# Kernel optimization log

Measured on AMD Instinct MI355X. Metric: run time of the kernel, lower is better.

## Reference

```python
import jax, jax.numpy as jnp
import numpy as np

DIM, M_DIM, FOURIER, KNN = 128, 16, 4, 32
EDGE_IN = 2 * FOURIER + 2 * DIM + 1  # 265


def silu(x):
    return x * jax.nn.sigmoid(x)


def setup_inputs() -> dict:
    key = jax.random.key(0)
    ks = jax.random.split(key, 12)
    b, n = 2, 4096

    def w(k, shape):
        return jax.random.normal(k, shape, dtype=jnp.float32) * 0.02

    return {
        "feats": jax.random.normal(ks[0], (b, n, DIM), dtype=jnp.float32),
        "coors": jax.random.normal(ks[1], (b, n, 3), dtype=jnp.float32) * 3.0,
        # edge_mlp: Linear(265, 530) -> SiLU -> Linear(530, 16) -> SiLU
        "We1": w(ks[2], (EDGE_IN, 2 * EDGE_IN)), "be1": jnp.zeros((2 * EDGE_IN,), jnp.float32),
        "We2": w(ks[3], (2 * EDGE_IN, M_DIM)), "be2": jnp.zeros((M_DIM,), jnp.float32),
        # coors_mlp: Linear(16, 64) -> SiLU -> Linear(64, 1)
        "Wc1": w(ks[4], (M_DIM, 4 * M_DIM)), "bc1": jnp.zeros((4 * M_DIM,), jnp.float32),
        "Wc2": w(ks[5], (4 * M_DIM, 1)), "bc2": jnp.zeros((1,), jnp.float32),
        # node_mlp: Linear(dim+16, 2*dim) -> SiLU -> Linear(2*dim, dim)
        "Wn1": w(ks[6], (DIM + M_DIM, 2 * DIM)), "bn1": jnp.zeros((2 * DIM,), jnp.float32),
        "Wn2": w(ks[7], (2 * DIM, DIM)), "bn2": jnp.zeros((DIM,), jnp.float32),
    }


def reference(feats, coors, We1, be1, We2, be2, Wc1, bc1, Wc2, bc2, Wn1, bn1, Wn2, bn2):
    b, n, d = feats.shape
    # pairwise relative coords and squared distance: (b, n, n, 3), (b, n, n)
    rel_coors = coors[:, :, None, :] - coors[:, None, :, :]
    rel_dist = jnp.sum(rel_coors ** 2, axis=-1)

    # k nearest neighbors (smallest distance)
    _, idx = jax.lax.top_k(-rel_dist, KNN)  # (b, n, K)
    rel_coors = jnp.take_along_axis(rel_coors, idx[..., None], axis=2)  # (b, n, K, 3)
    rel_dist = jnp.take_along_axis(rel_dist, idx, axis=2)[..., None]    # (b, n, K, 1)

    # fourier encode distance -> (b, n, K, 2*F + 1)
    scales = 2.0 ** jnp.arange(FOURIER, dtype=rel_dist.dtype)
    xs = rel_dist[..., None] / scales  # (b, n, K, 1, F)
    fe = jnp.concatenate([jnp.sin(xs), jnp.cos(xs), rel_dist[..., None]], axis=-1)
    rel_dist = fe.reshape(b, n, KNN, 2 * FOURIER + 1)

    bidx = jnp.arange(b)[:, None, None]
    feats_j = feats[bidx, idx]                                   # (b, n, K, d)
    feats_i = jnp.broadcast_to(feats[:, :, None, :], (b, n, KNN, d))

    edge_in = jnp.concatenate([feats_i, feats_j, rel_dist], axis=-1)  # (b, n, K, 265)
    m_ij = silu(silu(edge_in @ We1 + be1) @ We2 + be2)                # (b, n, K, m)

    coor_w = (silu(m_ij @ Wc1 + bc1) @ Wc2 + bc2)[..., 0]             # (b, n, K)
    coors_out = jnp.einsum('bij,bijc->bic', coor_w, rel_coors) + coors

    m_i = m_ij.sum(axis=2)                                            # (b, n, m)
    node_h = silu(jnp.concatenate([feats, m_i], axis=-1) @ Wn1 + bn1)
    node_out = node_h @ Wn2 + bn2 + feats
    return node_out, coors_out
```

## Files before the change

### kernel.cpp

```cpp
#include <hip/hip_runtime.h>
#include <hip/hip_bf16.h>
#include <stdint.h>

typedef __hip_bfloat16 bf16;

using sh8    = __attribute__((ext_vector_type(8)))  short;
using sh4    = __attribute__((ext_vector_type(4)))  short;
using us4    = __attribute__((ext_vector_type(4)))  unsigned short;
using f32x16 = __attribute__((ext_vector_type(16))) float;
using fx4    = __attribute__((ext_vector_type(4)))  float;
using i32x2  = __attribute__((ext_vector_type(2)))  int;

#define NN    4096
#define NODES 8192
#define DIM   128
#define MD    16
#define KNNK  32
#define H1N   530
#define CPAD  544
#define PROW  1088

#define OFF_W1AB 0
#define OFF_WE2A 8704
#define OFF_WC1A 17536
#define OFF_BE2  19584
#define OFF_BC1  19616
#define OFF_WC2  19744
#define OFF_BC2  19872
#define WIMG_SH  19880

__device__ __forceinline__ float b2f(bf16 x){ return __bfloat162float(x); }
__device__ __forceinline__ bf16  f2b(float x){ return __float2bfloat16(x); }
__device__ __forceinline__ float silu_f(float x){
    return x * __builtin_amdgcn_rcpf(1.f + __expf(-x));
}

__device__ __forceinline__ unsigned short f2us(float f){
    unsigned x = __float_as_uint(f);
    unsigned r = x + 0x7FFFu + ((x >> 16) & 1u);
    return (unsigned short)(r >> 16);
}
__device__ __forceinline__ float us2f(unsigned short u){
    return __uint_as_float(((unsigned)u) << 16);
}
__device__ __forceinline__ unsigned pkbf(float a, float b){
    __hip_bfloat162 v = __float22bfloat162_rn(make_float2(a, b));
    return *(unsigned*)&v;
}
__device__ __forceinline__ void plswap(unsigned &a, unsigned &b){
    i32x2 r = __builtin_amdgcn_permlane32_swap((int)a, (int)b, false, false);
    a = (unsigned)r[0]; b = (unsigned)r[1];
}
__device__ __forceinline__ sh8 mk8(unsigned a, unsigned b, unsigned c, unsigned d){
    union { unsigned u[4]; sh8 s; } x;
    x.u[0] = a; x.u[1] = b; x.u[2] = c; x.u[3] = d;
    return x.s;
}
__device__ __forceinline__ float ldconv(const void* p, int fl, size_t i){
    return fl ? ((const float*)p)[i] : b2f(((const bf16*)p)[i]);
}

struct Ptrs { const void* p[14]; int n[14]; };

__global__ __launch_bounds__(256) void detect_kernel(Ptrs ps, int* flags){
    int tn = blockIdx.x;
    const bf16* s = (const bf16*)ps.p[tn];
    int n = ps.n[tn]; if (n > 8192) n = 8192;
    int bad = 0;
    for (int i = threadIdx.x; i < n; i += 256){
        float v = b2f(s[i]);
        if (!(fabsf(v) <= 64.f)) bad = 1;
    }
    __shared__ int sbad;
    if (threadIdx.x == 0) sbad = 0;
    __syncthreads();
    if (bad) atomicOr(&sbad, 1);
    __syncthreads();
    if (threadIdx.x == 0) flags[tn] = sbad;
}

#define PREP_TOTAL 1315776
__global__ __launch_bounds__(256) void prep_all(Ptrs ps, const int* __restrict__ flags,
        unsigned short* __restrict__ gwimg, unsigned short* __restrict__ We1T,
        unsigned short* __restrict__ fBF,   float* __restrict__ coorsF,
        float* __restrict__ be1F,  float* __restrict__ Wn1F,
        float* __restrict__ bn1F,  float* __restrict__ Wn2F,
        float* __restrict__ bn2F){
    int gid = blockIdx.x * 256 + threadIdx.x;
    if (gid < 4352){
        int c = gid >> 3, f = gid & 7;
        gwimg[OFF_W1AB + gid] =
            (c < H1N) ? f2us(ldconv(ps.p[2], flags[2], (size_t)(256 + f) * H1N + c)) : 0;
    } else if (gid < 8704){
        int e = gid - 4352; int c = e >> 3, jj = e & 7;
        gwimg[OFF_W1AB + 4352 + e] =
            (jj == 0 && c < H1N) ? f2us(ldconv(ps.p[2], flags[2], (size_t)264 * H1N + c)) : 0;
    } else if (gid < 17536){
        int e = gid - 8704; int o = e / 552, c = e - o * 552;
        gwimg[OFF_WE2A + e] =
            (c < H1N) ? f2us(ldconv(ps.p[4], flags[4], (size_t)c * 16 + o)) : 0;
    } else if (gid < 19584){
        int e = gid - 17536; int u = e >> 5, k = e & 31;
        gwimg[OFF_WC1A + e] =
            (k < 16) ? f2us(ldconv(ps.p[6], flags[6], (size_t)k * 64 + u)) : 0;
    } else if (gid < 19600){
        ((float*)(gwimg + OFF_BE2))[gid - 19584] = ldconv(ps.p[5], flags[5], gid - 19584);
    } else if (gid < 19664){
        ((float*)(gwimg + OFF_BC1))[gid - 19600] = ldconv(ps.p[7], flags[7], gid - 19600);
    } else if (gid < 19728){
        ((float*)(gwimg + OFF_WC2))[gid - 19664] = ldconv(ps.p[8], flags[8], gid - 19664);
    } else if (gid < 19732){
        int z = gid - 19728;
        ((float*)(gwimg + OFF_BC2))[z] = (z == 0) ? ldconv(ps.p[9], flags[9], 0) : 0.f;
    } else if (gid >= 32768 && gid < 172032){
        int e = gid - 32768; int n = e >> 7, k = e & 127;
        float v;
        if (n < CPAD) v = (n < H1N) ? ldconv(ps.p[2], flags[2], (size_t)k * H1N + n) : 0.f;
        else { int n2 = n - CPAD;
               v = (n2 < H1N) ? ldconv(ps.p[2], flags[2], (size_t)(128 + k) * H1N + n2) : 0.f; }
        We1T[e] = f2us(v);
    } else if (gid >= 172032 && gid < 1220608){
        int e = gid - 172032;
        fBF[e] = f2us(ldconv(ps.p[0], flags[0], e));
    } else if (gid >= 1220608 && gid < 1245184){
        int e = gid - 1220608;
        coorsF[e] = ldconv(ps.p[1], flags[1], e);
    } else if (gid >= 1245184 && gid < 1245714){
        int e = gid - 1245184;
        be1F[e] = ldconv(ps.p[3], flags[3], e);
    } else if (gid >= 1245760 && gid < 1282624){
        int e = gid - 1245760;
        Wn1F[e] = ldconv(ps.p[10], flags[10], e);
    } else if (gid >= 1282624 && gid < 1282880){
        int e = gid - 1282624;
        bn1F[e] = ldconv(ps.p[11], flags[11], e);
    } else if (gid >= 1282880 && gid < 1315648){
        int e = gid - 1282880;
        Wn2F[e] = ldconv(ps.p[12], flags[12], e);
    } else if (gid >= 1315648 && gid < 1315776){
        int e = gid - 1315648;
        bn2F[e] = ldconv(ps.p[13], flags[13], e);
    }
}

__global__ __launch_bounds__(512, 6) void knn_pgemm(
        const float* __restrict__ coors, int* __restrict__ idx_out,
        const unsigned short* __restrict__ fBF,
        const unsigned short* __restrict__ We1T,
        const float* __restrict__ be1, unsigned short* __restrict__ P){
    __shared__ unsigned hist[8][1024];
    __shared__ unsigned long long blist[8][64];
    __shared__ int cntO[8], cntB[8];

    int bid = blockIdx.x;
    int t = threadIdx.x, lane = t & 63, wid = t >> 6;
    int e31 = lane & 31, hi = lane >> 5;

    bool is_knn = (bid < 2048) && !(bid & 1);
    int sub = (bid < 2048) ? (bid >> 1) : (bid - 1024);

    if (!is_knn){
        int bx = sub & 63, by = sub >> 6;
        int mW = (bx << 7) + ((wid & 3) << 5);
        int n0 = (by << 6) + ((wid >> 2) << 5);

        const unsigned short* Arow = fBF  + (size_t)(mW + e31) * DIM + hi * 8;
        const unsigned short* Brow = We1T + (size_t)(n0 + e31) * DIM + hi * 8;

        f32x16 acc = {0.f,0.f,0.f,0.f,0.f,0.f,0.f,0.f,0.f,0.f,0.f,0.f,0.f,0.f,0.f,0.f};
        #pragma unroll
        for (int kc = 0; kc < 8; ++kc){
            sh8 a  = *(const sh8*)(Arow + kc * 16);
            sh8 bv = *(const sh8*)(Brow + kc * 16);
            acc = __builtin_amdgcn_mfma_f32_32x32x16_bf16(a, bv, acc, 0, 0, 0);
        }
        int n = n0 + e31;
        float beadd = 0.f;
        if (n < CPAD) beadd = (n < H1N) ? be1[n] : 0.f;
        #pragma unroll
        for (int g = 0; g < 4; ++g)
            #pragma unroll
            for (int r = 0; r < 4; ++r){
                int m = mW + 8*g + 4*hi + r;
                P[(size_t)m * PROW + n] = f2us(acc[4*g + r] + beadd);
            }
        return;
    }

    int node = (sub << 3) + wid;
    int b = node >> 12, i = node & (NN - 1);
    const float* cb = coors + (size_t)b * NN * 3;

    float qx = cb[i*3+0], qy = cb[i*3+1], qz = cb[i*3+2];

    unsigned* h = &hist[wid][0];
    {
        uint4* hz = (uint4*)h;
        uint4 z = make_uint4(0,0,0,0);
        #pragma unroll
        for (int zl = 0; zl < 4; ++zl) hz[zl * 64 + lane] = z;
    }
    if (lane == 0){ cntO[wid] = 0; cntB[wid] = 0; }
    asm volatile("" ::: "memory");

    #pragma unroll 4
    for (int s = 0; s < 64; ++s){
        int j = (s << 6) + lane;
        float dx = qx - cb[j*3+0];
        float dy = qy - cb[j*3+1];
        float dz = qz - cb[j*3+2];
        float d  = dx*dx + dy*dy + dz*dz;
        float d2 = d * d;
        atomicAdd(&h[__float_as_uint(d2 * d2) >> 22], 1u);
    }
    asm volatile("s_waitcnt lgkmcnt(0)" ::: "memory");

    unsigned S = 0;
    {
        uint4* hz = (uint4*)h;
        #pragma unroll
        for (int g = 0; g < 4; ++g){
            uint4 v = hz[lane * 4 + g];
            S += v.x + v.y + v.z + v.w;
        }
    }
    unsigned scan = S;
    #pragma unroll
    for (int off = 1; off < 64; off <<= 1){
        unsigned nv = __shfl_up(scan, off);
        if (lane >= off) scan += nv;
    }
    unsigned excl = scan - S;
    unsigned long long own = __ballot(excl < KNNK && excl + S >= KNNK);
    int src = __ffsll((unsigned long long)own) - 1;
    unsigned run = excl, Bloc = 0, below_l = 0;
    #pragma unroll
    for (int r = 0; r < 16; ++r){
        unsigned c = h[lane * 16 + r];
        if (run < KNNK && run + c >= KNNK){ Bloc = lane * 16 + r; below_l = run; }
        run += c;
    }
    unsigned B    = __shfl(Bloc, src);
    unsigned below= __shfl(below_l, src);
    unsigned need = KNNK - below;

    int* co = &cntO[wid];
    int* cbn = &cntB[wid];
    unsigned long long* bl = &blist[wid][0];
    #pragma unroll 4
    for (int s = 0; s < 64; ++s){
        int j = (s << 6) + lane;
        float dx = qx - cb[j*3+0];
        float dy = qy - cb[j*3+1];
        float dz = qz - cb[j*3+2];
        float d  = dx*dx + dy*dy + dz*dz;
        float d2 = d * d;
        unsigned bk = __float_as_uint(d2 * d2) >> 22;
        if (bk < B){
            int pos = atomicAdd(co, 1);
            idx_out[(size_t)node * KNNK + pos] = j;
        } else if (bk == B){
            unsigned long long mk = ((unsigned long long)__float_as_uint(d) << 32)
                                    | (unsigned)j;
            int p = atomicAdd(cbn, 1);
            if (p < 64) bl[p] = mk;
        }
    }
    asm volatile("s_waitcnt lgkmcnt(0) vmcnt(0)" ::: "memory");
    int nb = *cbn;

    if (nb <= 64){
        unsigned long long e = (lane < nb) ? bl[lane] : ~0ull;
        for (unsigned r = 0; r < need; ++r){
            unsigned long long m = e;
            #pragma unroll
            for (int off = 32; off > 0; off >>= 1){
                unsigned long long o = __shfl_xor(m, off);
                if (o < m) m = o;
            }
            if (lane == 0)
                idx_out[(size_t)node * KNNK + below + r] = (int)(unsigned)(m & 0xffffffffull);
            if (e == m) e = ~0ull;
        }
    } else {
        unsigned long long lastk = 0;
        for (unsigned r = 0; r < need; ++r){
            unsigned long long lmin = ~0ull;
            for (int s = 0; s < 64; ++s){
                int j = (s << 6) + lane;
                float dx = qx - cb[j*3+0];
                float dy = qy - cb[j*3+1];
                float dz = qz - cb[j*3+2];
                float d  = dx*dx + dy*dy + dz*dz;
                float d2 = d * d;
                if ((__float_as_uint(d2 * d2) >> 22) == B){
                    unsigned long long mk = (((unsigned long long)__float_as_uint(d) << 32)
                                             | (unsigned)j) + 1ull;
                    if (mk > lastk && mk < lmin) lmin = mk;
                }
            }
            #pragma unroll
            for (int off = 32; off > 0; off >>= 1){
                unsigned long long o = __shfl_xor(lmin, off);
                if (o < lmin) lmin = o;
            }
            if (lane == 0)
                idx_out[(size_t)node * KNNK + below + r] =
                    (int)(unsigned)((lmin - 1ull) & 0xffffffffull);
            lastk = lmin;
        }
    }
}

__global__ __launch_bounds__(512, 6) void edge_kernel(
        const float* __restrict__ coors, const int* __restrict__ idx,
        const unsigned short* __restrict__ gw,
        const unsigned short* __restrict__ P,
        float* __restrict__ mi_out, void* __restrict__ dout,
        const int* __restrict__ flagp){
    __shared__ __align__(16) unsigned short sWe2[16 * 552];
    __shared__ __align__(16) unsigned short trans[8][1280];

    int t = threadIdx.x, lane = t & 63, wid = t >> 6;
    int gnode = (blockIdx.x << 3) + wid;
    int b = gnode >> 12;

    {
        const float4* s1 = (const float4*)(gw + OFF_WE2A);
        float4* d1 = (float4*)sWe2;
        for (int e = t; e < 1104; e += 512) d1[e] = s1[e];
    }

    const float* cb = coors + (size_t)b * NN * 3;
    int i = gnode & (NN - 1);
    float qx = cb[i*3+0], qy = cb[i*3+1], qz = cb[i*3+2];

    int e31 = lane & 31, hi = lane >> 5;
    int e15 = lane & 15, q  = lane >> 4;

    int jme = idx[(size_t)gnode * KNNK + e31];
    float rx = qx - cb[jme*3+0];
    float ry = qy - cb[jme*3+1];
    float rz = qz - cb[jme*3+2];
    float d = rx*rx + ry*ry + rz*rz;

    float s8v, c8v;
    __sincosf(d * 0.125f, &s8v, &c8v);
    float s4  = 2.f*s8v*c8v, c4  = 1.f - 2.f*s8v*s8v;
    float s2a = 2.f*s4*c4,   c2a = 1.f - 2.f*s4*s4;
    float s1a = 2.f*s2a*c2a, c1a = 1.f - 2.f*s2a*s2a;

    unsigned frb[9];
    frb[0] = f2us(s1a); frb[1] = f2us(s2a); frb[2] = f2us(s4); frb[3] = f2us(s8v);
    frb[4] = f2us(c1a); frb[5] = f2us(c2a); frb[6] = f2us(c4); frb[7] = f2us(c8v);
    frb[8] = f2us(d);

    sh8 bfragC;
    #pragma unroll
    for (int j = 0; j < 8; ++j)
        bfragC[j] = (hi == 0) ? (short)frb[j]
                  : (short)((j == 0) ? frb[8] : (j == 1) ? 0x3F80u : 0u);

    int nbase = gnode & ~(NN - 1);
    int j0 = __shfl(jme, lane >> 2);
    int j1 = __shfl(jme, 16 + (lane >> 2));
    const unsigned short* Pst0 = P + (size_t)(nbase + j0) * PROW + CPAD + (lane & 3) * 8;
    const unsigned short* Pst1 = P + (size_t)(nbase + j1) * PROW + CPAD + (lane & 3) * 8;
    const unsigned short* Pirow = P + (size_t)gnode * PROW;

    unsigned short* stg = &trans[wid][0];
    unsigned short* sw0 = stg + (lane >> 2) * 40 + (lane & 3) * 8;
    unsigned short* sw1 = stg + (16 + (lane >> 2)) * 40 + (lane & 3) * 8;

    const float* g_be2 = (const float*)(gw + OFF_BE2);
    const float* g_bc1 = (const float*)(gw + OFF_BC1);
    const float* g_wc2 = (const float*)(gw + OFF_WC2);
    const float* g_bc2 = (const float*)(gw + OFF_BC2);

    f32x16 accD = {0.f,0.f,0.f,0.f,0.f,0.f,0.f,0.f,
                   0.f,0.f,0.f,0.f,0.f,0.f,0.f,0.f};

    sh8 g0v = *(const sh8*)(Pst0);
    sh8 g1v = *(const sh8*)(Pst1);

    __syncthreads();

    #pragma unroll 1
    for (int ch = 0; ch < 17; ++ch){
        int c0 = ch * 32;
        *(sh8*)sw0 = g0v;
        *(sh8*)sw1 = g1v;
        if (ch < 16){
            g0v = *(const sh8*)(Pst0 + c0 + 32);
            g1v = *(const sh8*)(Pst1 + c0 + 32);
        }

        unsigned short piS = Pirow[c0 + e31];
        sh8 afrag = *(const sh8*)(gw + OFF_W1AB + (size_t)(hi * 544 + c0 + e31) * 8);
        afrag[1] = hi ? (short)piS : afrag[1];

        f32x16 cc;
        #pragma unroll
        for (int g = 0; g < 4; ++g){
            us4 pj = *(const us4*)(stg + e31 * 40 + 8*g + 4*hi);
            cc[4*g+0] = us2f(pj.x);
            cc[4*g+1] = us2f(pj.y);
            cc[4*g+2] = us2f(pj.z);
            cc[4*g+3] = us2f(pj.w);
        }
        f32x16 h = __builtin_amdgcn_mfma_f32_32x32x16_bf16(afrag, bfragC, cc, 0, 0, 0);

        unsigned u0 = pkbf(silu_f(h[0]),  silu_f(h[1]));
        unsigned u1 = pkbf(silu_f(h[2]),  silu_f(h[3]));
        unsigned u2 = pkbf(silu_f(h[4]),  silu_f(h[5]));
        unsigned u3 = pkbf(silu_f(h[6]),  silu_f(h[7]));
        unsigned u4 = pkbf(silu_f(h[8]),  silu_f(h[9]));
        unsigned u5 = pkbf(silu_f(h[10]), silu_f(h[11]));
        unsigned u6 = pkbf(silu_f(h[12]), silu_f(h[13]));
        unsigned u7 = pkbf(silu_f(h[14]), silu_f(h[15]));
        plswap(u0, u2); plswap(u1, u3);
        plswap(u4, u6); plswap(u5, u7);
        sh8 A1 = mk8(u0, u1, u2, u3);
        sh8 A2 = mk8(u4, u5, u6, u7);

        const unsigned short* wrow = &sWe2[(size_t)(e31 & 15) * 552 + c0 + (hi << 3)];
        sh8 B1 = *(const sh8*)(wrow);
        sh8 B2 = *(const sh8*)(wrow + 16);
        accD = __builtin_amdgcn_mfma_f32_32x32x16_bf16(A1, B1, accD, 0, 0, 0);
        accD = __builtin_amdgcn_mfma_f32_32x32x16_bf16(A2, B2, accD, 0, 0, 0);
    }

    float be2v = g_be2[e31 & 15];
    float mval[16];
    float msum = 0.f;
    #pragma unroll
    for (int r = 0; r < 16; ++r){
        mval[r] = silu_f(accD[r] + be2v);
        msum += mval[r];
    }
    msum += __shfl_xor(msum, 32);

    if (e31 < 16){
        #pragma unroll
        for (int r = 0; r < 16; ++r){
            int edge = (r & 3) + 8 * (r >> 2) + 4 * hi;
            stg[edge * 16 + e31] = f2us(mval[r]);
        }
        if (hi == 0)
            mi_out[(size_t)gnode * MD + e31] = msum;
    }

    float tsum0 = 0.f, tsum1 = 0.f;
    #pragma unroll
    for (int ut = 0; ut < 4; ++ut){
        sh8 wa3 = *(const sh8*)(gw + OFF_WC1A + (size_t)(ut * 16 + e15) * 32 + q * 8);
        sh8 b0  = (q < 2) ? *(const sh8*)&stg[e15 * 16 + q * 8]        : (sh8)0;
        sh8 b1  = (q < 2) ? *(const sh8*)&stg[(16 + e15) * 16 + q * 8] : (sh8)0;
        fx4 a0 = {0.f,0.f,0.f,0.f};
        fx4 a1 = {0.f,0.f,0.f,0.f};
        a0 = __builtin_amdgcn_mfma_f32_16x16x32_bf16(wa3, b0, a0, 0, 0, 0);
        a1 = __builtin_amdgcn_mfma_f32_16x16x32_bf16(wa3, b1, a1, 0, 0, 0);
        fx4 bc1q = *(const fx4*)&g_bc1[ut * 16 + q * 4];
        fx4 wcq  = *(const fx4*)&g_wc2[ut * 16 + q * 4];
        #pragma unroll
        for (int r = 0; r < 4; ++r){
            tsum0 += silu_f(a0[r] + bc1q[r]) * wcq[r];
            tsum1 += silu_f(a1[r] + bc1q[r]) * wcq[r];
        }
    }
    tsum0 += __shfl_xor(tsum0, 16); tsum0 += __shfl_xor(tsum0, 32);
    tsum1 += __shfl_xor(tsum1, 16); tsum1 += __shfl_xor(tsum1, 32);
    float cw = ((lane < 16) ? tsum0 : tsum1) + g_bc2[0];

    float en = (lane < 32) ? 1.f : 0.f;
    float cx = en * cw * rx, cy = en * cw * ry, cz = en * cw * rz;
    #pragma unroll
    for (int off = 1; off <= 32; off <<= 1){
        cx += __shfl_xor(cx, off);
        cy += __shfl_xor(cy, off);
        cz += __shfl_xor(cz, off);
    }
    if (lane == 0){
        size_t base = (size_t)NODES * DIM + (size_t)gnode * 3;
        if (*flagp){
            float* o = (float*)dout;
            o[base+0] = cx + qx; o[base+1] = cy + qy; o[base+2] = cz + qz;
        } else {
            bf16* o = (bf16*)dout;
            o[base+0] = f2b(cx + qx); o[base+1] = f2b(cy + qy); o[base+2] = f2b(cz + qz);
        }
    }
}

__global__ __launch_bounds__(256) void node_kernel(
        const void* __restrict__ featsRaw, const float* __restrict__ m_i,
        const float* __restrict__ Wn1,   const float* __restrict__ bn1,
        const float* __restrict__ Wn2,   const float* __restrict__ bn2,
        void* __restrict__ dout,         const int* __restrict__ flagp){
    __shared__ float X[8][144];
    __shared__ float Hs[8][256];
    int t = threadIdx.x;
    int g0 = blockIdx.x << 3;
    int fl = flagp[0];

    for (int e = t; e < 8 * DIM; e += 256){
        int nd = e >> 7, c = e & 127;
        size_t off = (size_t)(g0 + nd) * DIM + c;
        X[nd][c] = fl ? ((const float*)featsRaw)[off]
                      : b2f(((const bf16*)featsRaw)[off]);
    }
    if (t < 128){
        int nd = t >> 4, c = t & 15;
        X[nd][DIM + c] = m_i[(size_t)(g0 + nd) * MD + c];
    }
    __syncthreads();

    float acc[8] = {};
    for (int r = 0; r < 144; ++r){
        float w = Wn1[(size_t)r * 256 + t];
        #pragma unroll
        for (int nd = 0; nd < 8; ++nd) acc[nd] += X[nd][r] * w;
    }
    float bb = bn1[t];
    #pragma unroll
    for (int nd = 0; nd < 8; ++nd) Hs[nd][t] = silu_f(acc[nd] + bb);
    __syncthreads();

    int c = t & 127, g = t >> 7;
    float a2[4] = {};
    for (int r = 0; r < 256; ++r){
        float w = Wn2[(size_t)r * DIM + c];
        #pragma unroll
        for (int u = 0; u < 4; ++u) a2[u] += Hs[g*4 + u][r] * w;
    }
    float b2v = bn2[c];
    #pragma unroll
    for (int u = 0; u < 4; ++u){
        int nd = g*4 + u;
        float v = a2[u] + b2v + X[nd][c];
        size_t off2 = (size_t)(g0 + nd) * DIM + c;
        if (fl) ((float*)dout)[off2] = v;
        else    ((bf16*)dout)[off2]  = f2b(v);
    }
}

extern "C" void kernel_launch(void* const* d_in, const int* in_sizes, int n_in,
                              void* d_out, int out_size, void* d_ws, size_t ws_size,
                              hipStream_t stream){
    char* ws = (char*)d_ws;
    size_t off = 0;
    auto alloc = [&](size_t bytes) -> char* {
        off = (off + 511) & ~(size_t)511;
        char* p = ws + off;
        off += bytes;
        return p;
    };

    int* flags = (int*)alloc(14 * 4);
    unsigned short* gwimg = (unsigned short*)alloc((size_t)WIMG_SH * 2);
    unsigned short* We1T  = (unsigned short*)alloc((size_t)1088 * 128 * 2);
    unsigned short* fBF   = (unsigned short*)alloc((size_t)NODES * DIM * 2);
    float* coorsF = (float*)alloc((size_t)2 * NN * 3 * 4);
    float* be1F   = (float*)alloc((size_t)544 * 4);
    float* Wn1F   = (float*)alloc((size_t)144 * 256 * 4);
    float* bn1F   = (float*)alloc((size_t)256 * 4);
    float* Wn2F   = (float*)alloc((size_t)256 * 128 * 4);
    float* bn2F   = (float*)alloc((size_t)128 * 4);
    int*   idx    = (int*)  alloc((size_t)NODES * KNNK * 4);
    unsigned short* P = (unsigned short*) alloc((size_t)NODES * PROW * 2);
    float* mi     = (float*)alloc((size_t)NODES * MD * 4);

    Ptrs ps;
    for (int i = 0; i < 14; ++i){ ps.p[i] = d_in[i]; ps.n[i] = in_sizes[i]; }

    detect_kernel<<<14, 256, 0, stream>>>(ps, flags);
    prep_all<<<(PREP_TOTAL + 255) / 256, 256, 0, stream>>>(
        ps, flags, gwimg, We1T, fBF, coorsF, be1F, Wn1F, bn1F, Wn2F, bn2F);
    knn_pgemm<<<2112, 512, 0, stream>>>(coorsF, idx, fBF, We1T, be1F, P);
    edge_kernel<<<NODES/8, 512, 0, stream>>>(coorsF, idx, gwimg, P, mi,
                                             d_out, flags + 0);
    node_kernel<<<1024, 256, 0, stream>>>(d_in[0], mi, Wn1F, bn1F, Wn2F, bn2F,
                                          d_out, flags + 0);
}
```

Before: 272.3 us.

## Split fused kNN/projection kernel, use SoA coords with vector loads in kNN

Adds an SoA copy of the coordinates in the prep kernel so the kNN distance scans can use float4 loads along x, y and z instead of strided AoS loads. The interleaved kNN/P-GEMM kernel is split into a standalone kNN kernel and a separate MFMA projection GEMM launch. The node MLP inner loops are also unrolled by four with vectorised shared-memory reads. This gives up the overlap between the kNN and GEMM work inside one launch and adds an extra kernel launch, in exchange for simpler and better-coalesced memory access.

```diff
diff --git a/kernel.cpp b/kernel.cpp
--- a/kernel.cpp
+++ b/kernel.cpp
@@ -79,13 +79,13 @@
     if (threadIdx.x == 0) flags[tn] = sbad;
 }
 
-#define PREP_TOTAL 1315776
+#define PREP_TOTAL 1340352
 __global__ __launch_bounds__(256) void prep_all(Ptrs ps, const int* __restrict__ flags,
         unsigned short* __restrict__ gwimg, unsigned short* __restrict__ We1T,
         unsigned short* __restrict__ fBF,   float* __restrict__ coorsF,
         float* __restrict__ be1F,  float* __restrict__ Wn1F,
         float* __restrict__ bn1F,  float* __restrict__ Wn2F,
-        float* __restrict__ bn2F){
+        float* __restrict__ bn2F,  float* __restrict__ coorsS){
     int gid = blockIdx.x * 256 + threadIdx.x;
     if (gid < 4352){
         int c = gid >> 3, f = gid & 7;
@@ -140,58 +140,27 @@
     } else if (gid >= 1315648 && gid < 1315776){
         int e = gid - 1315648;
         bn2F[e] = ldconv(ps.p[13], flags[13], e);
-    }
-}
-
-__global__ __launch_bounds__(512, 6) void knn_pgemm(
-        const float* __restrict__ coors, int* __restrict__ idx_out,
-        const unsigned short* __restrict__ fBF,
-        const unsigned short* __restrict__ We1T,
-        const float* __restrict__ be1, unsigned short* __restrict__ P){
+    } else if (gid >= 1315776 && gid < 1340352){
+        int e = gid - 1315776;
+        int n = e / 3, c = e - n * 3;
+        coorsS[(size_t)c * NODES + n] = ldconv(ps.p[1], flags[1], e);
+    }
+}
+
+__global__ __launch_bounds__(512, 6) void knn_kernel(const float* __restrict__ coorsS,
+                                                     int* __restrict__ idx_out){
     __shared__ unsigned hist[8][1024];
     __shared__ unsigned long long blist[8][64];
     __shared__ int cntO[8], cntB[8];
 
-    int bid = blockIdx.x;
     int t = threadIdx.x, lane = t & 63, wid = t >> 6;
-    int e31 = lane & 31, hi = lane >> 5;
-
-    bool is_knn = (bid < 2048) && !(bid & 1);
-    int sub = (bid < 2048) ? (bid >> 1) : (bid - 1024);
-
-    if (!is_knn){
-        int bx = sub & 63, by = sub >> 6;
-        int mW = (bx << 7) + ((wid & 3) << 5);
-        int n0 = (by << 6) + ((wid >> 2) << 5);
-
-        const unsigned short* Arow = fBF  + (size_t)(mW + e31) * DIM + hi * 8;
-        const unsigned short* Brow = We1T + (size_t)(n0 + e31) * DIM + hi * 8;
-
-        f32x16 acc = {0.f,0.f,0.f,0.f,0.f,0.f,0.f,0.f,0.f,0.f,0.f,0.f,0.f,0.f,0.f,0.f};
-        #pragma unroll
-        for (int kc = 0; kc < 8; ++kc){
-            sh8 a  = *(const sh8*)(Arow + kc * 16);
-            sh8 bv = *(const sh8*)(Brow + kc * 16);
-            acc = __builtin_amdgcn_mfma_f32_32x32x16_bf16(a, bv, acc, 0, 0, 0);
-        }
-        int n = n0 + e31;
-        float beadd = 0.f;
-        if (n < CPAD) beadd = (n < H1N) ? be1[n] : 0.f;
-        #pragma unroll
-        for (int g = 0; g < 4; ++g)
-            #pragma unroll
-            for (int r = 0; r < 4; ++r){
-                int m = mW + 8*g + 4*hi + r;
-                P[(size_t)m * PROW + n] = f2us(acc[4*g + r] + beadd);
-            }
-        return;
-    }
-
-    int node = (sub << 3) + wid;
+    int node = (blockIdx.x << 3) + wid;
     int b = node >> 12, i = node & (NN - 1);
-    const float* cb = coors + (size_t)b * NN * 3;
-
-    float qx = cb[i*3+0], qy = cb[i*3+1], qz = cb[i*3+2];
+    const float* cx = coorsS + (size_t)b * NN;
+    const float* cy = coorsS + NODES + (size_t)b * NN;
+    const float* cz = coorsS + 2 * NODES + (size_t)b * NN;
+
+    float qx = cx[i], qy = cy[i], qz = cz[i];
 
     unsigned* h = &hist[wid][0];
     {
@@ -203,15 +172,18 @@
     if (lane == 0){ cntO[wid] = 0; cntB[wid] = 0; }
     asm volatile("" ::: "memory");
 
-    #pragma unroll 4
-    for (int s = 0; s < 64; ++s){
-        int j = (s << 6) + lane;
-        float dx = qx - cb[j*3+0];
-        float dy = qy - cb[j*3+1];
-        float dz = qz - cb[j*3+2];
-        float d  = dx*dx + dy*dy + dz*dz;
-        float d2 = d * d;
-        atomicAdd(&h[__float_as_uint(d2 * d2) >> 22], 1u);
+    for (int s = 0; s < 16; ++s){
+        int j0 = (s << 8) + (lane << 2);
+        fx4 X = *(const fx4*)(cx + j0);
+        fx4 Y = *(const fx4*)(cy + j0);
+        fx4 Z = *(const fx4*)(cz + j0);
+        #pragma unroll
+        for (int k = 0; k < 4; ++k){
+            float dx = qx - X[k], dy = qy - Y[k], dz = qz - Z[k];
+            float d  = dx*dx + dy*dy + dz*dz;
+            float d2 = d * d;
+            atomicAdd(&h[__float_as_uint(d2 * d2) >> 22], 1u);
+        }
     }
     asm volatile("s_waitcnt lgkmcnt(0)" ::: "memory");
 
@@ -247,23 +219,27 @@
     int* co = &cntO[wid];
     int* cbn = &cntB[wid];
     unsigned long long* bl = &blist[wid][0];
-    #pragma unroll 4
-    for (int s = 0; s < 64; ++s){
-        int j = (s << 6) + lane;
-        float dx = qx - cb[j*3+0];
-        float dy = qy - cb[j*3+1];
-        float dz = qz - cb[j*3+2];
-        float d  = dx*dx + dy*dy + dz*dz;
-        float d2 = d * d;
-        unsigned bk = __float_as_uint(d2 * d2) >> 22;
-        if (bk < B){
-            int pos = atomicAdd(co, 1);
-            idx_out[(size_t)node * KNNK + pos] = j;
-        } else if (bk == B){
-            unsigned long long mk = ((unsigned long long)__float_as_uint(d) << 32)
-                                    | (unsigned)j;
-            int p = atomicAdd(cbn, 1);
-            if (p < 64) bl[p] = mk;
+    for (int s = 0; s < 16; ++s){
+        int j0 = (s << 8) + (lane << 2);
+        fx4 X = *(const fx4*)(cx + j0);
+        fx4 Y = *(const fx4*)(cy + j0);
+        fx4 Z = *(const fx4*)(cz + j0);
+        #pragma unroll
+        for (int k = 0; k < 4; ++k){
+            float dx = qx - X[k], dy = qy - Y[k], dz = qz - Z[k];
+            float d  = dx*dx + dy*dy + dz*dz;
+            float d2 = d * d;
+            unsigned bk = __float_as_uint(d2 * d2) >> 22;
+            int j = j0 + k;
+            if (bk < B){
+                int pos = atomicAdd(co, 1);
+                idx_out[(size_t)node * KNNK + pos] = j;
+            } else if (bk == B){
+                unsigned long long mk = ((unsigned long long)__float_as_uint(d) << 32)
+                                        | (unsigned)j;
+                int p = atomicAdd(cbn, 1);
+                if (p < 64) bl[p] = mk;
+            }
         }
     }
     asm volatile("s_waitcnt lgkmcnt(0) vmcnt(0)" ::: "memory");
@@ -288,9 +264,9 @@
             unsigned long long lmin = ~0ull;
             for (int s = 0; s < 64; ++s){
                 int j = (s << 6) + lane;
-                float dx = qx - cb[j*3+0];
-                float dy = qy - cb[j*3+1];
-                float dz = qz - cb[j*3+2];
+                float dx = qx - cx[j];
+                float dy = qy - cy[j];
+                float dz = qz - cz[j];
                 float d  = dx*dx + dy*dy + dz*dz;
                 float d2 = d * d;
                 if ((__float_as_uint(d2 * d2) >> 22) == B){
@@ -312,6 +288,37 @@
     }
 }
 
+__global__ __launch_bounds__(256) void p_gemm(const unsigned short* __restrict__ fBF,
+                                              const unsigned short* __restrict__ We1T,
+                                              const float* __restrict__ be1,
+                                              unsigned short* __restrict__ P){
+    int t = threadIdx.x, lane = t & 63, wid = t >> 6;
+    int e31 = lane & 31, hi = lane >> 5;
+    int mW = (blockIdx.x << 7) + (wid << 5);
+    int n0 = blockIdx.y << 5;
+
+    const unsigned short* Arow = fBF  + (size_t)(mW + e31) * DIM + hi * 8;
+    const unsigned short* Brow = We1T + (size_t)(n0 + e31) * DIM + hi * 8;
+
+    f32x16 acc = {0.f,0.f,0.f,0.f,0.f,0.f,0.f,0.f,0.f,0.f,0.f,0.f,0.f,0.f,0.f,0.f};
+    #pragma unroll
+    for (int kc = 0; kc < 8; ++kc){
+        sh8 a  = *(const sh8*)(Arow + kc * 16);
+        sh8 bv = *(const sh8*)(Brow + kc * 16);
+        acc = __builtin_amdgcn_mfma_f32_32x32x16_bf16(a, bv, acc, 0, 0, 0);
+    }
+    int n = n0 + e31;
+    float beadd = 0.f;
+    if (n < CPAD) beadd = (n < H1N) ? be1[n] : 0.f;
+    #pragma unroll
+    for (int g = 0; g < 4; ++g)
+        #pragma unroll
+        for (int r = 0; r < 4; ++r){
+            int m = mW + 8*g + 4*hi + r;
+            P[(size_t)m * PROW + n] = f2us(acc[4*g + r] + beadd);
+        }
+}
+
 __global__ __launch_bounds__(512, 6) void edge_kernel(
         const float* __restrict__ coors, const int* __restrict__ idx,
         const unsigned short* __restrict__ gw,
@@ -497,8 +504,8 @@
         const float* __restrict__ Wn1,   const float* __restrict__ bn1,
         const float* __restrict__ Wn2,   const float* __restrict__ bn2,
         void* __restrict__ dout,         const int* __restrict__ flagp){
-    __shared__ float X[8][144];
-    __shared__ float Hs[8][256];
+    __shared__ __align__(16) float X[8][144];
+    __shared__ __align__(16) float Hs[8][256];
     int t = threadIdx.x;
     int g0 = blockIdx.x << 3;
     int fl = flagp[0];
@@ -516,10 +523,16 @@
     __syncthreads();
 
     float acc[8] = {};
-    for (int r = 0; r < 144; ++r){
-        float w = Wn1[(size_t)r * 256 + t];
-        #pragma unroll
-        for (int nd = 0; nd < 8; ++nd) acc[nd] += X[nd][r] * w;
+    for (int r4 = 0; r4 < 144; r4 += 4){
+        float w0 = Wn1[(size_t)(r4+0) * 256 + t];
+        float w1 = Wn1[(size_t)(r4+1) * 256 + t];
+        float w2 = Wn1[(size_t)(r4+2) * 256 + t];
+        float w3 = Wn1[(size_t)(r4+3) * 256 + t];
+        #pragma unroll
+        for (int nd = 0; nd < 8; ++nd){
+            fx4 x4 = *(const fx4*)&X[nd][r4];
+            acc[nd] += x4[0]*w0 + x4[1]*w1 + x4[2]*w2 + x4[3]*w3;
+        }
     }
     float bb = bn1[t];
     #pragma unroll
@@ -528,10 +541,16 @@
 
     int c = t & 127, g = t >> 7;
     float a2[4] = {};
-    for (int r = 0; r < 256; ++r){
-        float w = Wn2[(size_t)r * DIM + c];
-        #pragma unroll
-        for (int u = 0; u < 4; ++u) a2[u] += Hs[g*4 + u][r] * w;
+    for (int r4 = 0; r4 < 256; r4 += 4){
+        float w0 = Wn2[(size_t)(r4+0) * DIM + c];
+        float w1 = Wn2[(size_t)(r4+1) * DIM + c];
+        float w2 = Wn2[(size_t)(r4+2) * DIM + c];
+        float w3 = Wn2[(size_t)(r4+3) * DIM + c];
+        #pragma unroll
+        for (int u = 0; u < 4; ++u){
+            fx4 h4 = *(const fx4*)&Hs[g*4 + u][r4];
+            a2[u] += h4[0]*w0 + h4[1]*w1 + h4[2]*w2 + h4[3]*w3;
+        }
     }
     float b2v = bn2[c];
     #pragma unroll
@@ -566,6 +585,7 @@
     float* bn1F   = (float*)alloc((size_t)256 * 4);
     float* Wn2F   = (float*)alloc((size_t)256 * 128 * 4);
     float* bn2F   = (float*)alloc((size_t)128 * 4);
+    float* coorsS = (float*)alloc((size_t)3 * NODES * 4);
     int*   idx    = (int*)  alloc((size_t)NODES * KNNK * 4);
     unsigned short* P = (unsigned short*) alloc((size_t)NODES * PROW * 2);
     float* mi     = (float*)alloc((size_t)NODES * MD * 4);
@@ -575,8 +595,9 @@
 
     detect_kernel<<<14, 256, 0, stream>>>(ps, flags);
     prep_all<<<(PREP_TOTAL + 255) / 256, 256, 0, stream>>>(
-        ps, flags, gwimg, We1T, fBF, coorsF, be1F, Wn1F, bn1F, Wn2F, bn2F);
-    knn_pgemm<<<2112, 512, 0, stream>>>(coorsF, idx, fBF, We1T, be1F, P);
+        ps, flags, gwimg, We1T, fBF, coorsF, be1F, Wn1F, bn1F, Wn2F, bn2F, coorsS);
+    knn_kernel<<<NODES/8, 512, 0, stream>>>(coorsS, idx);
+    p_gemm<<<dim3(64, 34), 256, 0, stream>>>(fBF, We1T, be1F, P);
     edge_kernel<<<NODES/8, 512, 0, stream>>>(coorsF, idx, gwimg, P, mi,
                                              d_out, flags + 0);
     node_kernel<<<1024, 256, 0, stream>>>(d_in[0], mi, Wn1F, bn1F, Wn2F, bn2F,
```

Result: faster. 252.0 us (-7.5%).
